# Kernel tuning notes

Measured on AMD Instinct MI355X. Metric: run time of the kernel, lower is better.

The kernel has to match this reference:

```python
import jax, jax.numpy as jnp
import numpy as np

N = 20000   # nodes
E = 160000  # edges
G = 32      # graphs in the batch
IN_DIM, HID, OUT = 27, 512, 256


def _linear_init(key, fan_in, fan_out):
    s = 1.0 / np.sqrt(fan_in)
    return jax.random.uniform(key, (fan_in, fan_out), jnp.float32, -s, s)


def setup_inputs() -> dict:
    key = jax.random.key(0)
    ks = jax.random.split(key, 16)
    feature = jax.random.normal(ks[0], (N, IN_DIM), jnp.float32)
    edge_src = jax.random.randint(ks[1], (E,), 0, N, jnp.int32)
    edge_dst = jax.random.randint(ks[2], (E,), 0, N, jnp.int32)
    graph_ids = jnp.sort(jax.random.randint(ks[3], (N,), 0, G, jnp.int32))
    dims = [(IN_DIM, HID), (HID, HID), (HID, OUT)]
    inp = {
        "feature": feature,
        "edge_src": edge_src,
        "edge_dst": edge_dst,
        "graph_ids": graph_ids,
    }
    k = 4
    for l, (fi, fo) in enumerate(dims):
        inp[f"W_self{l}"] = _linear_init(ks[k], fi, fo); k += 1
        inp[f"W_neigh{l}"] = _linear_init(ks[k], fi, fo); k += 1
        inp[f"b{l}"] = jnp.zeros((fo,), jnp.float32)
    return inp


def _sage_layer(h, edge_src, edge_dst, inv_deg, W_self, W_neigh, b):
    # mean aggregation of in-neighbors (src -> dst), DGL SAGEConv 'mean'
    msg = h[edge_src]                                   # [E, F]
    agg = jax.ops.segment_sum(msg, edge_dst, num_segments=N) * inv_deg  # [N, F]
    return h @ W_self + agg @ W_neigh + b


def reference(feature, edge_src, edge_dst, graph_ids,
              W_self0, W_neigh0, b0,
              W_self1, W_neigh1, b1,
              W_self2, W_neigh2, b2):
    ones_e = jnp.ones((E,), jnp.float32)
    deg = jax.ops.segment_sum(ones_e, edge_dst, num_segments=N)
    inv_deg = (1.0 / jnp.maximum(deg, 1.0))[:, None]    # [N, 1]

    h = _sage_layer(feature, edge_src, edge_dst, inv_deg, W_self0, W_neigh0, b0)
    h = jax.nn.relu(h)
    h = _sage_layer(h, edge_src, edge_dst, inv_deg, W_self1, W_neigh1, b1)
    h = jax.nn.relu(h)
    h = _sage_layer(h, edge_src, edge_dst, inv_deg, W_self2, W_neigh2, b2)
    # last layer: no activation (encoding=False -> last_activation=None)

    # AvgPooling: per-graph mean of node features
    ones_n = jnp.ones((N,), jnp.float32)
    counts = jax.ops.segment_sum(ones_n, graph_ids, num_segments=G)
    hg = jax.ops.segment_sum(h, graph_ids, num_segments=G) / jnp.maximum(counts, 1.0)[:, None]
    return h, hg
```

## Files before the change

kernel.cpp:

```cpp
#include <hip/hip_runtime.h>

constexpr int NN   = 20000;
constexpr int NE   = 160000;
constexpr int NG   = 32;
constexpr int IN   = 27;
constexpr int HID  = 512;
constexpr int OUT  = 256;
constexpr int MPAD = 20096;
constexpr int MT   = MPAD / 128;

typedef unsigned short u16;
typedef __bf16 bf16x8 __attribute__((ext_vector_type(8)));
typedef float  f32x4  __attribute__((ext_vector_type(4)));
typedef u16    u16x4  __attribute__((ext_vector_type(4)));

__device__ __forceinline__ u16 f2b(float x) {
  __bf16 h = (__bf16)x;
  return __builtin_bit_cast(u16, h);
}
__device__ __forceinline__ float b2f(u16 u) {
  __bf16 h = __builtin_bit_cast(__bf16, u);
  return (float)h;
}

#define GLOBAL_AS __attribute__((address_space(1)))
#define LDS_AS    __attribute__((address_space(3)))
__device__ __forceinline__ void gload_lds16(const void* g, void* l) {
  __builtin_amdgcn_global_load_lds((const GLOBAL_AS void*)g, (LDS_AS void*)l, 16, 0, 0);
}

__global__ void k_deg(const int* __restrict__ dst, int* __restrict__ deg) {
  int e = blockIdx.x * 256 + threadIdx.x;
  if (e < NE) atomicAdd(&deg[dst[e]], 1);
}

__global__ void k_scan(const int* __restrict__ deg, int* __restrict__ rowptr,
                       int* __restrict__ cursor, float* __restrict__ invdeg) {
  constexpr int CH = 20;
  __shared__ int sdeg[1024 * CH];
  __shared__ int wsum[16];
  const int tid = threadIdx.x;
  for (int j = tid; j < 1024 * CH; j += 1024) sdeg[j] = (j < NN) ? deg[j] : 0;
  __syncthreads();
  const int i0 = tid * CH;
  int loc[CH];
  int sum = 0;
#pragma unroll
  for (int j = 0; j < CH; ++j) { loc[j] = sum; sum += sdeg[i0 + j]; }
  const int lane = tid & 63, wv = tid >> 6;
  int incl = sum;
#pragma unroll
  for (int off = 1; off < 64; off <<= 1) {
    int n = __shfl_up(incl, off);
    if (lane >= off) incl += n;
  }
  if (lane == 63) wsum[wv] = incl;
  __syncthreads();
  if (tid == 0) {
    int s = 0;
#pragma unroll
    for (int w = 0; w < 16; ++w) { int v = wsum[w]; wsum[w] = s + v; s += v; }
  }
  __syncthreads();
  const int wbase = (wv == 0) ? 0 : wsum[wv - 1];
  const int tbase = wbase + incl - sum;
#pragma unroll
  for (int j = 0; j < CH; ++j) {
    const int i = i0 + j;
    if (i < NN) {
      const int excl = tbase + loc[j];
      const int d = sdeg[i];
      rowptr[i] = excl;
      cursor[i] = excl;
      invdeg[i] = 1.0f / fmaxf((float)d, 1.0f);
    }
  }
  if (tid == 0) rowptr[NN] = wsum[15];
}

__global__ void k_scatter(const int* __restrict__ src, const int* __restrict__ dst,
                          int* __restrict__ cursor, int* __restrict__ ssrc) {
  int e = blockIdx.x * 256 + threadIdx.x;
  if (e < NE) {
    int p = atomicAdd(&cursor[dst[e]], 1);
    ssrc[p] = src[e];
  }
}

constexpr int WC0 = 512 * 64;
constexpr int WC1 = 512 * 1024;
constexpr int WC2 = 256 * 1024;
constexpr int WCT = WC0 + WC1 + WC2;
__global__ void k_wconv_all(const float* __restrict__ Ws0, const float* __restrict__ Wn0,
                            const float* __restrict__ Ws1, const float* __restrict__ Wn1,
                            const float* __restrict__ Ws2, const float* __restrict__ Wn2,
                            u16* __restrict__ Bt0, u16* __restrict__ Bt1,
                            u16* __restrict__ BtSN2) {
  int idx = blockIdx.x * 256 + threadIdx.x;
  if (idx < WC0) {
    const int n = idx / 64, k = idx % 64;
    float v = 0.0f;
    if (k < IN)           v = Ws0[(size_t)k * 512 + n];
    else if (k < 2 * IN)  v = Wn0[(size_t)(k - IN) * 512 + n];
    Bt0[idx] = f2b(v);
    return;
  }
  idx -= WC0;
  if (idx < WC1) {
    const int n = idx / 1024, k = idx % 1024;
    const float v = (k < 512) ? Ws1[(size_t)k * 512 + n] : Wn1[(size_t)(k - 512) * 512 + n];
    Bt1[idx] = f2b(v);
    return;
  }
  idx -= WC1;
  if (idx < WC2) {
    const int n = idx / 1024, k = idx % 1024;
    const float v = (k < 512) ? Ws2[(size_t)k * 256 + n] : Wn2[(size_t)(k - 512) * 256 + n];
    BtSN2[idx] = f2b(v);
  }
}

__global__ void k_build_A0(const float* __restrict__ feat, const int* __restrict__ rowptr,
                           const int* __restrict__ ssrc, const float* __restrict__ invdeg,
                           u16* __restrict__ A0) {
  const int r = blockIdx.x, t = threadIdx.x;
  u16* row = A0 + (size_t)r * 64;
  if (r >= NN) { row[t] = 0; return; }
  if (t < IN) {
    row[t] = f2b(feat[(size_t)r * IN + t]);
    float s = 0.0f;
    const int e0 = rowptr[r], e1 = rowptr[r + 1];
    for (int e = e0; e < e1; ++e) s += feat[(size_t)ssrc[e] * IN + t];
    row[IN + t] = f2b(s * invdeg[r]);
  } else if (t >= 2 * IN) {
    row[t] = 0;
  }
}

__global__ void k_agg512(u16* __restrict__ X, const int* __restrict__ rowptr,
                         const int* __restrict__ ssrc, const float* __restrict__ invdeg) {
  const int r = blockIdx.x, t = threadIdx.x;
  float a0 = 0, a1 = 0, a2 = 0, a3 = 0;
  const int e0 = rowptr[r], e1 = rowptr[r + 1];
  for (int e = e0; e < e1; ++e) {
    const u16x4 v = *(const u16x4*)(X + (size_t)ssrc[e] * 1024 + t * 4);
    a0 += b2f(v.x); a1 += b2f(v.y); a2 += b2f(v.z); a3 += b2f(v.w);
  }
  const float inv = invdeg[r];
  u16x4 o; o.x = f2b(a0 * inv); o.y = f2b(a1 * inv); o.z = f2b(a2 * inv); o.w = f2b(a3 * inv);
  *(u16x4*)(X + (size_t)r * 1024 + 512 + t * 4) = o;
}

__global__ __launch_bounds__(256) void k_gemm(
    const u16* __restrict__ A, int lda,
    const u16* __restrict__ Bt, int K,
    void* __restrict__ Out, int ldo,
    const float* __restrict__ bias,
    int flags, int nt) {
  __shared__ u16 As[128 * 64];
  __shared__ u16 Bs[128 * 64];
  const int tid = threadIdx.x;
  const int wid = tid >> 6, lane = tid & 63;
  const int l16 = lane & 15, lhi = lane >> 4;
  const int wr = wid >> 1, wc = wid & 1;

  const int G    = gridDim.x;
  const int PER  = nt * 8;
  const int nOct = G / PER;
  const int base = nOct * PER;
  int x, y;
  if ((int)blockIdx.x < base) {
    x = (blockIdx.x & 7) + 8 * (blockIdx.x / PER);
    y = (blockIdx.x >> 3) & (nt - 1);
  } else {
    const int j = blockIdx.x - base;
    x = 8 * nOct + j / nt;
    y = j - (j / nt) * nt;
  }
  const int row0 = x * 128, col0 = y * 128;

  const int tr    = tid >> 3;
  const int slot  = tid & 7;
  const int sslot = slot ^ (tr & 7);

  f32x4 acc[4][4] = {};

  for (int kt = 0; kt < K; kt += 64) {
#pragma unroll
    for (int i = 0; i < 4; ++i) {
      const int r = i * 32 + tr;
      gload_lds16(A  + (size_t)(row0 + r) * lda + kt + sslot * 8, &As[i * 2048 + wid * 512]);
      gload_lds16(Bt + (size_t)(col0 + r) * K   + kt + sslot * 8, &Bs[i * 2048 + wid * 512]);
    }
    __syncthreads();
#pragma unroll
    for (int ks = 0; ks < 2; ++ks) {
      bf16x8 af[4], bfr[4];
#pragma unroll
      for (int i = 0; i < 4; ++i) {
        const int r = wr * 64 + i * 16 + l16;
        const int s = (ks * 4 + lhi) ^ (r & 7);
        af[i] = *(const bf16x8*)&As[r * 64 + s * 8];
      }
#pragma unroll
      for (int n = 0; n < 4; ++n) {
        const int c = wc * 64 + n * 16 + l16;
        const int s = (ks * 4 + lhi) ^ (c & 7);
        bfr[n] = *(const bf16x8*)&Bs[c * 64 + s * 8];
      }
#pragma unroll
      for (int i = 0; i < 4; ++i)
#pragma unroll
        for (int n = 0; n < 4; ++n)
          acc[i][n] = __builtin_amdgcn_mfma_f32_16x16x32_bf16(af[i], bfr[n], acc[i][n], 0, 0, 0);
    }
    __syncthreads();
  }

  const bool relu = flags & 1;
  const bool f32o = flags & 2;
#pragma unroll
  for (int i = 0; i < 4; ++i) {
#pragma unroll
    for (int n = 0; n < 4; ++n) {
      const int C = col0 + wc * 64 + n * 16 + l16;
      const float bv = bias ? bias[C] : 0.0f;
#pragma unroll
      for (int q = 0; q < 4; ++q) {
        const int R = row0 + wr * 64 + i * 16 + lhi * 4 + q;
        float v = acc[i][n][q] + bv;
        if (f32o) {
          if (R < NN) ((float*)Out)[(size_t)R * ldo + C] = v;
        } else {
          if (relu) v = fmaxf(v, 0.0f);
          ((u16*)Out)[(size_t)R * ldo + C] = f2b(v);
        }
      }
    }
  }
}

__device__ __forceinline__ int lower_bound_g(const int* __restrict__ gid, int g) {
  int lo = 0, hi = NN;
  while (lo < hi) {
    const int mid = (lo + hi) >> 1;
    if (gid[mid] < g) lo = mid + 1; else hi = mid;
  }
  return lo;
}
__global__ void k_pool(const float* __restrict__ h, const int* __restrict__ gid,
                       float* __restrict__ hg) {
  __shared__ int s_n0, s_n1;
  const int g = blockIdx.x >> 3, s = blockIdx.x & 7;
  const int t = threadIdx.x;
  if (t == 0) { s_n0 = lower_bound_g(gid, g); s_n1 = lower_bound_g(gid, g + 1); }
  __syncthreads();
  const int n0 = s_n0, n1 = s_n1;
  const int len = n1 - n0, chunk = (len + 7) / 8;
  const int a = n0 + s * chunk;
  const int b = min(a + chunk, n1);
  float acc = 0.0f;
  for (int i = a; i < b; ++i) acc += h[(size_t)i * 256 + t];
  if (b > a) {
    const float inv = 1.0f / fmaxf((float)len, 1.0f);
    atomicAdd(&hg[g * 256 + t], acc * inv);
  }
}

constexpr size_t OFF_A0    = 0;
constexpr size_t OFF_A1    = OFF_A0   + (size_t)MPAD * 64  * 2;
constexpr size_t OFF_A2    = OFF_A1   + (size_t)MPAD * 1024 * 2;
constexpr size_t OFF_BT0   = OFF_A2   + (size_t)MPAD * 1024 * 2;
constexpr size_t OFF_BT1   = OFF_BT0  + (size_t)512 * 64 * 2;
constexpr size_t OFF_BTSN2 = OFF_BT1  + (size_t)512 * 1024 * 2;
constexpr size_t OFF_DEG   = OFF_BTSN2+ (size_t)256 * 1024 * 2;
constexpr size_t OFF_RP    = OFF_DEG  + (size_t)NN * 4;
constexpr size_t OFF_CUR   = OFF_RP   + (size_t)(NN + 2) * 4;
constexpr size_t OFF_SSRC  = OFF_CUR  + (size_t)NN * 4;
constexpr size_t OFF_INVD  = OFF_SSRC + (size_t)NE * 4;

extern "C" void kernel_launch(void* const* d_in, const int* in_sizes, int n_in,
                              void* d_out, int out_size, void* d_ws, size_t ws_size,
                              hipStream_t stream) {
  const float* feature = (const float*)d_in[0];
  const int*   esrc    = (const int*)d_in[1];
  const int*   edst    = (const int*)d_in[2];
  const int*   gid     = (const int*)d_in[3];
  const float* Ws0 = (const float*)d_in[4],  *Wn0 = (const float*)d_in[5],  *b0 = (const float*)d_in[6];
  const float* Ws1 = (const float*)d_in[7],  *Wn1 = (const float*)d_in[8],  *b1 = (const float*)d_in[9];
  const float* Ws2 = (const float*)d_in[10], *Wn2 = (const float*)d_in[11], *b2 = (const float*)d_in[12];

  char* ws = (char*)d_ws;
  u16*   A0    = (u16*)  (ws + OFF_A0);
  u16*   A1    = (u16*)  (ws + OFF_A1);
  u16*   A2    = (u16*)  (ws + OFF_A2);
  u16*   Bt0   = (u16*)  (ws + OFF_BT0);
  u16*   Bt1   = (u16*)  (ws + OFF_BT1);
  u16*   BtSN2 = (u16*)  (ws + OFF_BTSN2);
  int*   deg   = (int*)  (ws + OFF_DEG);
  int*   rp    = (int*)  (ws + OFF_RP);
  int*   cur   = (int*)  (ws + OFF_CUR);
  int*   ssrc  = (int*)  (ws + OFF_SSRC);
  float* invd  = (float*)(ws + OFF_INVD);

  float* out_h  = (float*)d_out;
  float* out_hg = out_h + (size_t)NN * OUT;

  hipMemsetAsync(deg,  0, (size_t)NN * 4, stream);
  hipMemsetAsync(out_hg, 0, (size_t)NG * OUT * 4, stream);

  k_deg    <<<(NE + 255) / 256, 256, 0, stream>>>(edst, deg);
  k_scan   <<<1, 1024, 0, stream>>>(deg, rp, cur, invd);
  k_scatter<<<(NE + 255) / 256, 256, 0, stream>>>(esrc, edst, cur, ssrc);

  k_wconv_all<<<(WCT + 255) / 256, 256, 0, stream>>>(Ws0, Wn0, Ws1, Wn1, Ws2, Wn2,
                                                     Bt0, Bt1, BtSN2);

  k_build_A0<<<MPAD, 64, 0, stream>>>(feature, rp, ssrc, invd, A0);
  k_gemm<<<MT * 4, 256, 0, stream>>>(A0, 64, Bt0, 64, A1, 1024, b0, 1, 4);

  k_agg512<<<NN, 128, 0, stream>>>(A1, rp, ssrc, invd);
  k_gemm<<<MT * 4, 256, 0, stream>>>(A1, 1024, Bt1, 1024, A2, 1024, b1, 1, 4);

  k_agg512<<<NN, 128, 0, stream>>>(A2, rp, ssrc, invd);
  k_gemm<<<MT * 2, 256, 0, stream>>>(A2, 1024, BtSN2, 1024, out_h, 256, b2, 2, 2);

  k_pool<<<NG * 8, 256, 0, stream>>>(out_h, gid, out_hg);
}
```

Baseline: 313.2 us.

## Double-buffer GEMM LDS tiles to overlap global loads with MFMA

The GEMM kernel now keeps two LDS stages for the A and B tiles. It issues the direct-to-LDS loads for the next K tile before computing on the current one, waiting on vmcnt so only the older loads must finish. This is meant to hide global-memory latency behind the MFMA work. In exchange, LDS use per block doubles to 64KB, which may lower occupancy. The hand-written waitcnt/barrier sequence also carries a correctness risk if the outstanding-load count of 8 does not match what the compiler emits.

```diff
diff --git a/kernel.cpp b/kernel.cpp
--- a/kernel.cpp
+++ b/kernel.cpp
@@ -157,8 +157,7 @@
     void* __restrict__ Out, int ldo,
     const float* __restrict__ bias,
     int flags, int nt) {
-  __shared__ u16 As[128 * 64];
-  __shared__ u16 Bs[128 * 64];
+  __shared__ u16 Sbuf[2][2][128 * 64];
   const int tid = threadIdx.x;
   const int wid = tid >> 6, lane = tid & 63;
   const int l16 = lane & 15, lhi = lane >> 4;
@@ -183,16 +182,32 @@
   const int slot  = tid & 7;
   const int sslot = slot ^ (tr & 7);
 
-  f32x4 acc[4][4] = {};
-
-  for (int kt = 0; kt < K; kt += 64) {
+  auto STAGE = [&](int kt, u16* as, u16* bs) {
 #pragma unroll
     for (int i = 0; i < 4; ++i) {
       const int r = i * 32 + tr;
-      gload_lds16(A  + (size_t)(row0 + r) * lda + kt + sslot * 8, &As[i * 2048 + wid * 512]);
-      gload_lds16(Bt + (size_t)(col0 + r) * K   + kt + sslot * 8, &Bs[i * 2048 + wid * 512]);
-    }
-    __syncthreads();
+      gload_lds16(A  + (size_t)(row0 + r) * lda + kt + sslot * 8, &as[i * 2048 + wid * 512]);
+      gload_lds16(Bt + (size_t)(col0 + r) * K   + kt + sslot * 8, &bs[i * 2048 + wid * 512]);
+    }
+  };
+
+  f32x4 acc[4][4] = {};
+  const int nsteps = K >> 6;
+  int cur = 0;
+
+  STAGE(0, &Sbuf[0][0][0], &Sbuf[0][1][0]);
+
+  for (int t = 0; t < nsteps; ++t) {
+    if (t + 1 < nsteps) {
+      STAGE((t + 1) << 6, &Sbuf[cur ^ 1][0][0], &Sbuf[cur ^ 1][1][0]);
+      asm volatile("s_waitcnt vmcnt(8)" ::: "memory");
+    } else {
+      asm volatile("s_waitcnt vmcnt(0)" ::: "memory");
+    }
+    asm volatile("s_barrier" ::: "memory");
+
+    const u16* as = &Sbuf[cur][0][0];
+    const u16* bs = &Sbuf[cur][1][0];
 #pragma unroll
     for (int ks = 0; ks < 2; ++ks) {
       bf16x8 af[4], bfr[4];
@@ -200,13 +215,13 @@
       for (int i = 0; i < 4; ++i) {
         const int r = wr * 64 + i * 16 + l16;
         const int s = (ks * 4 + lhi) ^ (r & 7);
-        af[i] = *(const bf16x8*)&As[r * 64 + s * 8];
+        af[i] = *(const bf16x8*)&as[r * 64 + s * 8];
       }
 #pragma unroll
       for (int n = 0; n < 4; ++n) {
         const int c = wc * 64 + n * 16 + l16;
         const int s = (ks * 4 + lhi) ^ (c & 7);
-        bfr[n] = *(const bf16x8*)&Bs[c * 64 + s * 8];
+        bfr[n] = *(const bf16x8*)&bs[c * 64 + s * 8];
       }
 #pragma unroll
       for (int i = 0; i < 4; ++i)
@@ -214,7 +229,8 @@
         for (int n = 0; n < 4; ++n)
           acc[i][n] = __builtin_amdgcn_mfma_f32_16x16x32_bf16(af[i], bfr[n], acc[i][n], 0, 0, 0);
     }
-    __syncthreads();
+    asm volatile("s_barrier" ::: "memory");
+    cur ^= 1;
   }
 
   const bool relu = flags & 1;
```

Result: no change. 314.0 us (+0.2%).
